# Kernel tuning notes

Hardware: AMD Instinct MI355X
Metric: run time of the kernel (lower is better)

The kernel has to match this reference:

```python
import jax, jax.numpy as jnp
import numpy as np


def setup_inputs() -> dict:
    H = 2048          # code_size == decoder_size (required for output feedback)
    T = 512           # sentence_length
    key = jax.random.key(0)
    k = jax.random.split(key, 5)
    s = 1.0 / np.sqrt(H)  # PyTorch LSTM init range
    return {
        "X": jax.random.normal(k[0], (1, 1, H), dtype=jnp.float32),
        "W_ih": jax.random.uniform(k[1], (4 * H, H), jnp.float32, -s, s),
        "W_hh": jax.random.uniform(k[2], (4 * H, H), jnp.float32, -s, s),
        "b_ih": jax.random.uniform(k[3], (4 * H,), jnp.float32, -s, s),
        "b_hh": jax.random.uniform(k[4], (4 * H,), jnp.float32, -s, s),
        "sentence_length": T,
    }


def reference(X, W_ih, W_hh, b_ih, b_hh, sentence_length):
    # the previous output h. PyTorch gate order: i, f, g, o.
    H = W_hh.shape[1]
    x0 = X[0]                       # (1, H)  batch=1
    h0 = jnp.zeros((1, H), X.dtype)
    c0 = jnp.zeros((1, H), X.dtype)

    def step(carry, _):
        x, h, c = carry
        gates = x @ W_ih.T + b_ih + h @ W_hh.T + b_hh   # (1, 4H)
        i, f, g, o = jnp.split(gates, 4, axis=-1)
        c_new = jax.nn.sigmoid(f) * c + jax.nn.sigmoid(i) * jnp.tanh(g)
        h_new = jax.nn.sigmoid(o) * jnp.tanh(c_new)
        # next step's input is this step's output (decoder feedback)
        return (h_new, h_new, c_new), h_new

    _, ys = jax.lax.scan(step, (x0, h0, c0), None, length=sentence_length)
    return ys  # (T, 1, H) == torch all_output
```

## Files before the change

kernel.cpp:

```cpp
#include <hip/hip_runtime.h>
#include <hip/hip_fp16.h>
#include <math.h>

#define HDIM 2048
#define G4   (4 * HDIM)
#define NBLK 128
#define TPB  512
#define NSLOT 1024

typedef __fp16 h2_t __attribute__((ext_vector_type(2)));

__device__ __forceinline__ float fast_sigmoid(float x) {
    return 1.0f / (1.0f + __expf(-x));
}
__device__ __forceinline__ float fast_tanh(float x) {
    return 1.0f - 2.0f / (1.0f + __expf(2.0f * x));
}
__device__ __forceinline__ h2_t pk2(float a, float b) {
#if __has_builtin(__builtin_amdgcn_cvt_pkrtz)
    return __builtin_amdgcn_cvt_pkrtz(a, b);
#else
    return h2_t{(__fp16)a, (__fp16)b};
#endif
}

__global__ __launch_bounds__(256) void prep_slots(unsigned long long* __restrict__ slots) {
    int i = blockIdx.x * blockDim.x + threadIdx.x;
    if (i < 2 * NSLOT) slots[i] = 0ull;
}

__global__ __launch_bounds__(256) void prep_small(const float* __restrict__ bih,
                                                  const float* __restrict__ bhh,
                                                  float* __restrict__ bsum,
                                                  float* __restrict__ c) {
    int i = blockIdx.x * blockDim.x + threadIdx.x;
    if (i < G4) bsum[i] = bih[i] + bhh[i];
    if (i < HDIM) c[i] = 0.0f;
}

__global__ __launch_bounds__(256) void prep_wsum_h(const float* __restrict__ Wih,
                                                   const float* __restrict__ Whh,
                                                   __half* __restrict__ Wsum) {
    const int n8 = (G4 * HDIM) / 8;
    int idx = blockIdx.x * blockDim.x + threadIdx.x;
    int stride = gridDim.x * blockDim.x;
    const float4* a = (const float4*)Wih;
    const float4* b = (const float4*)Whh;
    for (int i = idx; i < n8; i += stride) {
        float4 a0 = a[2 * i], a1 = a[2 * i + 1];
        float4 b0 = b[2 * i], b1 = b[2 * i + 1];
        __half h[8];
        h[0] = __float2half(a0.x + b0.x);
        h[1] = __float2half(a0.y + b0.y);
        h[2] = __float2half(a0.z + b0.z);
        h[3] = __float2half(a0.w + b0.w);
        h[4] = __float2half(a1.x + b1.x);
        h[5] = __float2half(a1.y + b1.y);
        h[6] = __float2half(a1.z + b1.z);
        h[7] = __float2half(a1.w + b1.w);
        ((uint4*)Wsum)[i] = *(const uint4*)h;
    }
}

__global__ __launch_bounds__(256) void lstm_step_f32(const float* __restrict__ x,
                                                     const float* __restrict__ W,
                                                     const float* __restrict__ bsum,
                                                     float* __restrict__ c,
                                                     float* __restrict__ h_out) {
    __shared__ float gates[4][8];
    const int tid  = threadIdx.x;
    const int wave = tid >> 6;
    const int lane = tid & 63;
    const int j0   = blockIdx.x * 8;

    float4 xv[8];
    const float4* xp = (const float4*)x;
#pragma unroll
    for (int k = 0; k < 8; ++k) xv[k] = xp[lane + 64 * k];

    float acc[8];
#pragma unroll
    for (int j8 = 0; j8 < 8; ++j8) {
        const int R = wave * HDIM + j0 + j8;
        const float4* wr = (const float4*)(W + (size_t)R * HDIM);
        float a = 0.0f;
#pragma unroll
        for (int k = 0; k < 8; ++k) {
            float4 wv = wr[lane + 64 * k];
            a += wv.x * xv[k].x + wv.y * xv[k].y + wv.z * xv[k].z + wv.w * xv[k].w;
        }
        acc[j8] = a;
    }
#pragma unroll
    for (int j8 = 0; j8 < 8; ++j8) {
        float a = acc[j8];
#pragma unroll
        for (int off = 32; off > 0; off >>= 1) a += __shfl_down(a, off, 64);
        if (lane == 0) gates[wave][j8] = a + bsum[wave * HDIM + j0 + j8];
    }
    __syncthreads();
    if (tid < 8) {
        const int j = j0 + tid;
        const float si = 1.0f / (1.0f + expf(-gates[0][tid]));
        const float so = 1.0f / (1.0f + expf(-gates[3][tid]));
        const float tg = tanhf(gates[2][tid]);
        const float cn = si * tg;
        c[j]     = cn;
        h_out[j] = so * tanhf(cn);
    }
}

__global__ __launch_bounds__(256) void lstm_step_h(const float* __restrict__ x,
                                                   const __half* __restrict__ W,
                                                   const float* __restrict__ bsum,
                                                   float* __restrict__ c,
                                                   float* __restrict__ h_out) {
    __shared__ float gates[4][8];
    const int tid  = threadIdx.x;
    const int wave = tid >> 6;
    const int lane = tid & 63;
    const int j0   = blockIdx.x * 8;

    float xv[32];
    const float4* xp = (const float4*)x;
#pragma unroll
    for (int k = 0; k < 4; ++k) {
        float4 a = xp[k * 128 + lane * 2];
        float4 b = xp[k * 128 + lane * 2 + 1];
        xv[k * 8 + 0] = a.x; xv[k * 8 + 1] = a.y; xv[k * 8 + 2] = a.z; xv[k * 8 + 3] = a.w;
        xv[k * 8 + 4] = b.x; xv[k * 8 + 5] = b.y; xv[k * 8 + 6] = b.z; xv[k * 8 + 7] = b.w;
    }
    float acc[8];
#pragma unroll
    for (int j8 = 0; j8 < 8; ++j8) {
        const int R = wave * HDIM + j0 + j8;
        const uint4* wr = (const uint4*)(W + (size_t)R * HDIM);
        float a = 0.0f;
#pragma unroll
        for (int k = 0; k < 4; ++k) {
            uint4 wv = wr[k * 64 + lane];
            const __half* hh = (const __half*)&wv;
#pragma unroll
            for (int e = 0; e < 8; ++e)
                a = fmaf(__half2float(hh[e]), xv[k * 8 + e], a);
        }
        acc[j8] = a;
    }
#pragma unroll
    for (int j8 = 0; j8 < 8; ++j8) {
        float a = acc[j8];
#pragma unroll
        for (int off = 32; off > 0; off >>= 1) a += __shfl_down(a, off, 64);
        if (lane == 0) gates[wave][j8] = a + bsum[wave * HDIM + j0 + j8];
    }
    __syncthreads();
    if (tid < 8) {
        const int j = j0 + tid;
        const float si = 1.0f / (1.0f + expf(-gates[0][tid]));
        const float sf = 1.0f / (1.0f + expf(-gates[1][tid]));
        const float so = 1.0f / (1.0f + expf(-gates[3][tid]));
        const float tg = tanhf(gates[2][tid]);
        const float cn = sf * c[j] + si * tg;
        c[j]     = cn;
        h_out[j] = so * tanhf(cn);
    }
}

__global__ __launch_bounds__(TPB, 2) void lstm_persist(const float* __restrict__ X,
                                                       const float* __restrict__ Wih,
                                                       const float* __restrict__ Whh,
                                                       const float* __restrict__ bih,
                                                       const float* __restrict__ bhh,
                                                       float* __restrict__ out,
                                                       unsigned long long* __restrict__ slots,
                                                       int T) {
    const int tid  = threadIdx.x;
    const int wave = tid >> 6;
    const int lane = tid & 63;
    const int jA   = blockIdx.x * 16 + 2 * wave;

    if (wave == 0) __builtin_amdgcn_s_setprio(1);

    float xv[32];
    {
        const float4* xp = (const float4*)X;
#pragma unroll
        for (int e = 0; e < 4; ++e) {
            float4 a = xp[(lane + 64 * e) * 2];
            float4 b = xp[(lane + 64 * e) * 2 + 1];
            xv[e * 8 + 0] = a.x; xv[e * 8 + 1] = a.y; xv[e * 8 + 2] = a.z; xv[e * 8 + 3] = a.w;
            xv[e * 8 + 4] = b.x; xv[e * 8 + 5] = b.y; xv[e * 8 + 6] = b.z; xv[e * 8 + 7] = b.w;
        }
    }

    uint4 w[8][4];
    float bias[8], acc[8];
#pragma unroll
    for (int g = 0; g < 4; ++g)
#pragma unroll
        for (int q = 0; q < 2; ++q) {
            const int j8 = g * 2 + q;
            const size_t R = (size_t)g * HDIM + jA + q;
            const float4* ri = (const float4*)(Wih + R * HDIM);
            const float4* rh = (const float4*)(Whh + R * HDIM);
            float a0acc = 0.0f;
#pragma unroll
            for (int e = 0; e < 4; ++e) {
                float4 a0 = ri[(lane + 64 * e) * 2];
                float4 a1 = ri[(lane + 64 * e) * 2 + 1];
                float4 b0 = rh[(lane + 64 * e) * 2];
                float4 b1 = rh[(lane + 64 * e) * 2 + 1];
                a0acc += a0.x * xv[e * 8 + 0] + a0.y * xv[e * 8 + 1]
                       + a0.z * xv[e * 8 + 2] + a0.w * xv[e * 8 + 3]
                       + a1.x * xv[e * 8 + 4] + a1.y * xv[e * 8 + 5]
                       + a1.z * xv[e * 8 + 6] + a1.w * xv[e * 8 + 7];
                h2_t p0 = pk2(a0.x + b0.x, a0.y + b0.y);
                h2_t p1 = pk2(a0.z + b0.z, a0.w + b0.w);
                h2_t p2 = pk2(a1.x + b1.x, a1.y + b1.y);
                h2_t p3 = pk2(a1.z + b1.z, a1.w + b1.w);
                w[j8][e] = make_uint4(__builtin_bit_cast(unsigned, p0),
                                      __builtin_bit_cast(unsigned, p1),
                                      __builtin_bit_cast(unsigned, p2),
                                      __builtin_bit_cast(unsigned, p3));
            }
            acc[j8]  = a0acc;
            bias[j8] = bih[R] + bhh[R];
        }

    __shared__ __align__(16) unsigned lds_x[2][NSLOT];
    __shared__ unsigned h_pack[8];
    __shared__ float h_outf[16];

    float cA = 0.0f, cB = 0.0f;

#pragma unroll
    for (int j8 = 0; j8 < 8; ++j8)
#pragma unroll
        for (int off = 32; off > 0; off >>= 1)
            acc[j8] += __shfl_xor(acc[j8], off, 64);
    {
        const float iA = fast_sigmoid(acc[0] + bias[0]);
        const float iB = fast_sigmoid(acc[1] + bias[1]);
        const float gA = fast_tanh(acc[4] + bias[4]);
        const float gB = fast_tanh(acc[5] + bias[5]);
        const float oA = fast_sigmoid(acc[6] + bias[6]);
        const float oB = fast_sigmoid(acc[7] + bias[7]);
        cA = iA * gA;
        cB = iB * gB;
        const float hA = oA * fast_tanh(cA);
        const float hB = oB * fast_tanh(cB);
        if (lane == 0) {
            h_pack[wave] = __builtin_bit_cast(unsigned, pk2(hA, hB));
            h_outf[2 * wave]     = hA;
            h_outf[2 * wave + 1] = hB;
        }
    }
    __syncthreads();
    if (wave == 0 && lane < 8) {
        unsigned long long pkv = (1ull << 32) | (unsigned long long)h_pack[lane];
        __hip_atomic_store(&slots[blockIdx.x * 8 + lane], pkv,
                           __ATOMIC_RELAXED, __HIP_MEMORY_SCOPE_AGENT);
    }

    for (int t = 1; t < T; ++t) {
        if (wave == 1 && lane < 16) {
            out[(size_t)(t - 1) * HDIM + blockIdx.x * 16 + lane] = h_outf[lane];
        }

        const int buf = (t - 1) & 1;
        const unsigned long long* sl = slots + (size_t)buf * NSLOT;
        const unsigned tg = (unsigned)t;
        const int s0 = wave * 128 + lane;
        const int s1 = s0 + 64;
        unsigned long long v0 = __hip_atomic_load(&sl[s0], __ATOMIC_RELAXED,
                                                  __HIP_MEMORY_SCOPE_AGENT);
        unsigned long long v1 = __hip_atomic_load(&sl[s1], __ATOMIC_RELAXED,
                                                  __HIP_MEMORY_SCOPE_AGENT);
        int spin = 0;
        while (((unsigned)(v0 >> 32) != tg) | ((unsigned)(v1 >> 32) != tg)) {
            if (spin++) __builtin_amdgcn_s_sleep(1);
            if ((unsigned)(v0 >> 32) != tg)
                v0 = __hip_atomic_load(&sl[s0], __ATOMIC_RELAXED,
                                       __HIP_MEMORY_SCOPE_AGENT);
            if ((unsigned)(v1 >> 32) != tg)
                v1 = __hip_atomic_load(&sl[s1], __ATOMIC_RELAXED,
                                       __HIP_MEMORY_SCOPE_AGENT);
        }
        lds_x[buf][s0] = (unsigned)v0;
        lds_x[buf][s1] = (unsigned)v1;
        __syncthreads();

        float a2[8] = {0.f, 0.f, 0.f, 0.f, 0.f, 0.f, 0.f, 0.f};
#pragma unroll
        for (int e = 0; e < 4; ++e) {
            const uint4 xq = *(const uint4*)&lds_x[buf][(lane + 64 * e) * 4];
            const unsigned xs[4] = {xq.x, xq.y, xq.z, xq.w};
#pragma unroll
            for (int p = 0; p < 4; ++p) {
                const h2_t xh = __builtin_bit_cast(h2_t, xs[p]);
#pragma unroll
                for (int j8 = 0; j8 < 8; ++j8) {
                    const h2_t* wh = (const h2_t*)&w[j8][e];
#if __has_builtin(__builtin_amdgcn_fdot2)
                    a2[j8] = __builtin_amdgcn_fdot2(wh[p], xh, a2[j8], false);
#else
                    a2[j8] = fmaf((float)wh[p][0], (float)xh[0],
                                  fmaf((float)wh[p][1], (float)xh[1], a2[j8]));
#endif
                }
            }
        }

#pragma unroll
        for (int j8 = 0; j8 < 8; ++j8)
#pragma unroll
            for (int off = 32; off > 0; off >>= 1)
                a2[j8] += __shfl_xor(a2[j8], off, 64);

        const float iA = fast_sigmoid(a2[0] + bias[0]);
        const float iB = fast_sigmoid(a2[1] + bias[1]);
        const float fA = fast_sigmoid(a2[2] + bias[2]);
        const float fB = fast_sigmoid(a2[3] + bias[3]);
        const float gA = fast_tanh(a2[4] + bias[4]);
        const float gB = fast_tanh(a2[5] + bias[5]);
        const float oA = fast_sigmoid(a2[6] + bias[6]);
        const float oB = fast_sigmoid(a2[7] + bias[7]);
        cA = fA * cA + iA * gA;
        cB = fB * cB + iB * gB;
        const float hA = oA * fast_tanh(cA);
        const float hB = oB * fast_tanh(cB);

        if (lane == 0) {
            h_pack[wave] = __builtin_bit_cast(unsigned, pk2(hA, hB));
            h_outf[2 * wave]     = hA;
            h_outf[2 * wave + 1] = hB;
        }
        __syncthreads();

        if (wave == 0 && lane < 8) {
            unsigned long long pkv = ((unsigned long long)(unsigned)(t + 1) << 32)
                                   | (unsigned long long)h_pack[lane];
            __hip_atomic_store(&slots[(size_t)(t & 1) * NSLOT + blockIdx.x * 8 + lane],
                               pkv, __ATOMIC_RELAXED, __HIP_MEMORY_SCOPE_AGENT);
        }
    }

    if (wave == 1 && lane < 16) {
        out[(size_t)(T - 1) * HDIM + blockIdx.x * 16 + lane] = h_outf[lane];
    }
}

extern "C" void kernel_launch(void* const* d_in, const int* in_sizes, int n_in,
                              void* d_out, int out_size, void* d_ws, size_t ws_size,
                              hipStream_t stream) {
    const float* X   = (const float*)d_in[0];
    const float* Wih = (const float*)d_in[1];
    const float* Whh = (const float*)d_in[2];
    const float* bih = (const float*)d_in[3];
    const float* bhh = (const float*)d_in[4];
    float* out = (float*)d_out;

    int T = out_size / HDIM;

    const size_t wsum_bytes = (size_t)G4 * HDIM * sizeof(__half);
    char* ws = (char*)d_ws;
    __half* Wsum = (__half*)ws;
    float*  bsum = (float*)(ws + wsum_bytes);
    float*  c    = bsum + G4;
    unsigned long long* slots = (unsigned long long*)(c + HDIM);

    prep_slots<<<8, 256, 0, stream>>>(slots);

    void* args[] = {(void*)&X, (void*)&Wih, (void*)&Whh, (void*)&bih,
                    (void*)&bhh, (void*)&out, (void*)&slots, (void*)&T};
    hipError_t err = hipLaunchCooperativeKernel((const void*)lstm_persist,
                                                dim3(NBLK), dim3(TPB), args, 0, stream);
    if (err != hipSuccess) {
        prep_small<<<(G4 + 255) / 256, 256, 0, stream>>>(bih, bhh, bsum, c);
        prep_wsum_h<<<2048, 256, 0, stream>>>(Wih, Whh, Wsum);
        lstm_step_f32<<<256, 256, 0, stream>>>(X, Wih, bsum, c, out);
        for (int t = 1; t < T; ++t) {
            const float* hprev = out + (size_t)(t - 1) * HDIM;
            float* hnext = out + (size_t)t * HDIM;
            lstm_step_h<<<256, 256, 0, stream>>>(hprev, Wsum, bsum, c, hnext);
        }
    }
}
```

Measured before the change: 1.767 ms.

## Use 1024-thread blocks with one hidden unit per wave in persistent LSTM

Doubles the block size to 16 waves so each wave owns a single hidden unit (four gate rows) instead of two, halving the per-wave register weight storage and per-step fdot2 and reduction work. Each thread now polls exactly one flag slot instead of two, and the fp16 h values are packed in pairs from shared memory before publishing. The cost is a larger workgroup with more waves to synchronise at each __syncthreads, and occupancy limited to one block per CU.

```diff
diff --git a/kernel.cpp b/kernel.cpp
--- a/kernel.cpp
+++ b/kernel.cpp
@@ -5,7 +5,7 @@
 #define HDIM 2048
 #define G4   (4 * HDIM)
 #define NBLK 128
-#define TPB  512
+#define TPB  1024
 #define NSLOT 1024
 
 typedef __fp16 h2_t __attribute__((ext_vector_type(2)));
@@ -166,7 +166,7 @@
     }
 }
 
-__global__ __launch_bounds__(TPB, 2) void lstm_persist(const float* __restrict__ X,
+__global__ __launch_bounds__(TPB, 1) void lstm_persist(const float* __restrict__ X,
                                                        const float* __restrict__ Wih,
                                                        const float* __restrict__ Whh,
                                                        const float* __restrict__ bih,
@@ -177,7 +177,7 @@
     const int tid  = threadIdx.x;
     const int wave = tid >> 6;
     const int lane = tid & 63;
-    const int jA   = blockIdx.x * 16 + 2 * wave;
+    const int jH   = blockIdx.x * 16 + wave;
 
     if (wave == 0) __builtin_amdgcn_s_setprio(1);
 
@@ -193,71 +193,64 @@
         }
     }
 
-    uint4 w[8][4];
-    float bias[8], acc[8];
+    uint4 w[4][4];
+    float bias[4], acc[4];
+#pragma unroll
+    for (int g = 0; g < 4; ++g) {
+        const size_t R = (size_t)g * HDIM + jH;
+        const float4* ri = (const float4*)(Wih + R * HDIM);
+        const float4* rh = (const float4*)(Whh + R * HDIM);
+        float a0acc = 0.0f;
+#pragma unroll
+        for (int e = 0; e < 4; ++e) {
+            float4 a0 = ri[(lane + 64 * e) * 2];
+            float4 a1 = ri[(lane + 64 * e) * 2 + 1];
+            float4 b0 = rh[(lane + 64 * e) * 2];
+            float4 b1 = rh[(lane + 64 * e) * 2 + 1];
+            a0acc += a0.x * xv[e * 8 + 0] + a0.y * xv[e * 8 + 1]
+                   + a0.z * xv[e * 8 + 2] + a0.w * xv[e * 8 + 3]
+                   + a1.x * xv[e * 8 + 4] + a1.y * xv[e * 8 + 5]
+                   + a1.z * xv[e * 8 + 6] + a1.w * xv[e * 8 + 7];
+            h2_t p0 = pk2(a0.x + b0.x, a0.y + b0.y);
+            h2_t p1 = pk2(a0.z + b0.z, a0.w + b0.w);
+            h2_t p2 = pk2(a1.x + b1.x, a1.y + b1.y);
+            h2_t p3 = pk2(a1.z + b1.z, a1.w + b1.w);
+            w[g][e] = make_uint4(__builtin_bit_cast(unsigned, p0),
+                                 __builtin_bit_cast(unsigned, p1),
+                                 __builtin_bit_cast(unsigned, p2),
+                                 __builtin_bit_cast(unsigned, p3));
+        }
+        acc[g]  = a0acc;
+        bias[g] = bih[R] + bhh[R];
+    }
+
+    __shared__ __align__(16) unsigned lds_x[2][NSLOT];
+    __shared__ unsigned short h16[16];
+    __shared__ float h_outf[16];
+
+    float cc = 0.0f;
+
 #pragma unroll
     for (int g = 0; g < 4; ++g)
 #pragma unroll
-        for (int q = 0; q < 2; ++q) {
-            const int j8 = g * 2 + q;
-            const size_t R = (size_t)g * HDIM + jA + q;
-            const float4* ri = (const float4*)(Wih + R * HDIM);
-            const float4* rh = (const float4*)(Whh + R * HDIM);
-            float a0acc = 0.0f;
-#pragma unroll
-            for (int e = 0; e < 4; ++e) {
-                float4 a0 = ri[(lane + 64 * e) * 2];
-                float4 a1 = ri[(lane + 64 * e) * 2 + 1];
-                float4 b0 = rh[(lane + 64 * e) * 2];
-                float4 b1 = rh[(lane + 64 * e) * 2 + 1];
-                a0acc += a0.x * xv[e * 8 + 0] + a0.y * xv[e * 8 + 1]
-                       + a0.z * xv[e * 8 + 2] + a0.w * xv[e * 8 + 3]
-                       + a1.x * xv[e * 8 + 4] + a1.y * xv[e * 8 + 5]
-                       + a1.z * xv[e * 8 + 6] + a1.w * xv[e * 8 + 7];
-                h2_t p0 = pk2(a0.x + b0.x, a0.y + b0.y);
-                h2_t p1 = pk2(a0.z + b0.z, a0.w + b0.w);
-                h2_t p2 = pk2(a1.x + b1.x, a1.y + b1.y);
-                h2_t p3 = pk2(a1.z + b1.z, a1.w + b1.w);
-                w[j8][e] = make_uint4(__builtin_bit_cast(unsigned, p0),
-                                      __builtin_bit_cast(unsigned, p1),
-                                      __builtin_bit_cast(unsigned, p2),
-                                      __builtin_bit_cast(unsigned, p3));
-            }
-            acc[j8]  = a0acc;
-            bias[j8] = bih[R] + bhh[R];
-        }
-
-    __shared__ __align__(16) unsigned lds_x[2][NSLOT];
-    __shared__ unsigned h_pack[8];
-    __shared__ float h_outf[16];
-
-    float cA = 0.0f, cB = 0.0f;
-
-#pragma unroll
-    for (int j8 = 0; j8 < 8; ++j8)
-#pragma unroll
         for (int off = 32; off > 0; off >>= 1)
-            acc[j8] += __shfl_xor(acc[j8], off, 64);
+            acc[g] += __shfl_xor(acc[g], off, 64);
     {
-        const float iA = fast_sigmoid(acc[0] + bias[0]);
-        const float iB = fast_sigmoid(acc[1] + bias[1]);
-        const float gA = fast_tanh(acc[4] + bias[4]);
-        const float gB = fast_tanh(acc[5] + bias[5]);
-        const float oA = fast_sigmoid(acc[6] + bias[6]);
-        const float oB = fast_sigmoid(acc[7] + bias[7]);
-        cA = iA * gA;
-        cB = iB * gB;
-        const float hA = oA * fast_tanh(cA);
-        const float hB = oB * fast_tanh(cB);
+        const float si = fast_sigmoid(acc[0] + bias[0]);
+        const float tg = fast_tanh(acc[2] + bias[2]);
+        const float so = fast_sigmoid(acc[3] + bias[3]);
+        cc = si * tg;
+        const float h = so * fast_tanh(cc);
         if (lane == 0) {
-            h_pack[wave] = __builtin_bit_cast(unsigned, pk2(hA, hB));
-            h_outf[2 * wave]     = hA;
-            h_outf[2 * wave + 1] = hB;
+            h16[wave] = (unsigned short)(__builtin_bit_cast(unsigned, pk2(h, h)) & 0xffffu);
+            h_outf[wave] = h;
         }
     }
     __syncthreads();
     if (wave == 0 && lane < 8) {
-        unsigned long long pkv = (1ull << 32) | (unsigned long long)h_pack[lane];
+        const unsigned payload = (unsigned)h16[2 * lane]
+                               | ((unsigned)h16[2 * lane + 1] << 16);
+        unsigned long long pkv = (1ull << 32) | (unsigned long long)payload;
         __hip_atomic_store(&slots[blockIdx.x * 8 + lane], pkv,
                            __ATOMIC_RELAXED, __HIP_MEMORY_SCOPE_AGENT);
     }
@@ -270,27 +263,19 @@
         const int buf = (t - 1) & 1;
         const unsigned long long* sl = slots + (size_t)buf * NSLOT;
         const unsigned tg = (unsigned)t;
-        const int s0 = wave * 128 + lane;
-        const int s1 = s0 + 64;
-        unsigned long long v0 = __hip_atomic_load(&sl[s0], __ATOMIC_RELAXED,
-                                                  __HIP_MEMORY_SCOPE_AGENT);
-        unsigned long long v1 = __hip_atomic_load(&sl[s1], __ATOMIC_RELAXED,
+
+        unsigned long long v0 = __hip_atomic_load(&sl[tid], __ATOMIC_RELAXED,
                                                   __HIP_MEMORY_SCOPE_AGENT);
         int spin = 0;
-        while (((unsigned)(v0 >> 32) != tg) | ((unsigned)(v1 >> 32) != tg)) {
+        while ((unsigned)(v0 >> 32) != tg) {
             if (spin++) __builtin_amdgcn_s_sleep(1);
-            if ((unsigned)(v0 >> 32) != tg)
-                v0 = __hip_atomic_load(&sl[s0], __ATOMIC_RELAXED,
-                                       __HIP_MEMORY_SCOPE_AGENT);
-            if ((unsigned)(v1 >> 32) != tg)
-                v1 = __hip_atomic_load(&sl[s1], __ATOMIC_RELAXED,
-                                       __HIP_MEMORY_SCOPE_AGENT);
-        }
-        lds_x[buf][s0] = (unsigned)v0;
-        lds_x[buf][s1] = (unsigned)v1;
+            v0 = __hip_atomic_load(&sl[tid], __ATOMIC_RELAXED,
+                                   __HIP_MEMORY_SCOPE_AGENT);
+        }
+        lds_x[buf][tid] = (unsigned)v0;
         __syncthreads();
 
-        float a2[8] = {0.f, 0.f, 0.f, 0.f, 0.f, 0.f, 0.f, 0.f};
+        float a2[4] = {0.f, 0.f, 0.f, 0.f};
 #pragma unroll
         for (int e = 0; e < 4; ++e) {
             const uint4 xq = *(const uint4*)&lds_x[buf][(lane + 64 * e) * 4];
@@ -299,47 +284,42 @@
             for (int p = 0; p < 4; ++p) {
                 const h2_t xh = __builtin_bit_cast(h2_t, xs[p]);
 #pragma unroll
-                for (int j8 = 0; j8 < 8; ++j8) {
-                    const h2_t* wh = (const h2_t*)&w[j8][e];
+                for (int g = 0; g < 4; ++g) {
+                    const h2_t* wh = (const h2_t*)&w[g][e];
 #if __has_builtin(__builtin_amdgcn_fdot2)
-                    a2[j8] = __builtin_amdgcn_fdot2(wh[p], xh, a2[j8], false);
+                    a2[g] = __builtin_amdgcn_fdot2(wh[p], xh, a2[g], false);
 #else
-                    a2[j8] = fmaf((float)wh[p][0], (float)xh[0],
-                                  fmaf((float)wh[p][1], (float)xh[1], a2[j8]));
+                    a2[g] = fmaf((float)wh[p][0], (float)xh[0],
+                                 fmaf((float)wh[p][1], (float)xh[1], a2[g]));
 #endif
                 }
             }
         }
 
 #pragma unroll
-        for (int j8 = 0; j8 < 8; ++j8)
+        for (int g = 0; g < 4; ++g)
 #pragma unroll
             for (int off = 32; off > 0; off >>= 1)
-                a2[j8] += __shfl_xor(a2[j8], off, 64);
-
-        const float iA = fast_sigmoid(a2[0] + bias[0]);
-        const float iB = fast_sigmoid(a2[1] + bias[1]);
-        const float fA = fast_sigmoid(a2[2] + bias[2]);
-        const float fB = fast_sigmoid(a2[3] + bias[3]);
-        const float gA = fast_tanh(a2[4] + bias[4]);
-        const float gB = fast_tanh(a2[5] + bias[5]);
-        const float oA = fast_sigmoid(a2[6] + bias[6]);
-        const float oB = fast_sigmoid(a2[7] + bias[7]);
-        cA = fA * cA + iA * gA;
-        cB = fB * cB + iB * gB;
-        const float hA = oA * fast_tanh(cA);
-        const float hB = oB * fast_tanh(cB);
+                a2[g] += __shfl_xor(a2[g], off, 64);
+
+        const float si = fast_sigmoid(a2[0] + bias[0]);
+        const float sf = fast_sigmoid(a2[1] + bias[1]);
+        const float tg2 = fast_tanh(a2[2] + bias[2]);
+        const float so = fast_sigmoid(a2[3] + bias[3]);
+        cc = sf * cc + si * tg2;
+        const float h = so * fast_tanh(cc);
 
         if (lane == 0) {
-            h_pack[wave] = __builtin_bit_cast(unsigned, pk2(hA, hB));
-            h_outf[2 * wave]     = hA;
-            h_outf[2 * wave + 1] = hB;
+            h16[wave] = (unsigned short)(__builtin_bit_cast(unsigned, pk2(h, h)) & 0xffffu);
+            h_outf[wave] = h;
         }
         __syncthreads();
 
         if (wave == 0 && lane < 8) {
+            const unsigned payload = (unsigned)h16[2 * lane]
+                                   | ((unsigned)h16[2 * lane + 1] << 16);
             unsigned long long pkv = ((unsigned long long)(unsigned)(t + 1) << 32)
-                                   | (unsigned long long)h_pack[lane];
+                                   | (unsigned long long)payload;
             __hip_atomic_store(&slots[(size_t)(t & 1) * NSLOT + blockIdx.x * 8 + lane],
                                pkv, __ATOMIC_RELAXED, __HIP_MEMORY_SCOPE_AGENT);
         }
```

New measurement: 1.657 ms. 1.07x faster.
